# Kernel tuning notes

Hardware: AMD Instinct MI355X
Metric: run time of the kernel (lower is better)

Reference implementation:

```python
import jax, jax.numpy as jnp
import numpy as np

NEG_SLOPE = 0.2  # PyG GATConv leaky_relu slope


def gat_conv(x, src, dst, W, a_src, a_dst, bias, heads, out_ch, concat, n_nodes):
    # x: [N, in], W: [heads*out_ch, in], a_src/a_dst: [heads, out_ch]
    h = (x @ W.T).reshape(n_nodes, heads, out_ch)          # [N,H,C]
    alpha_src = (h * a_src).sum(-1)                         # [N,H]
    alpha_dst = (h * a_dst).sum(-1)                         # [N,H]
    e = jax.nn.leaky_relu(alpha_src[src] + alpha_dst[dst], NEG_SLOPE)  # [E,H]
    # segment softmax over incoming edges of each dst node (self-loops ensure non-empty)
    m = jax.ops.segment_max(e, dst, num_segments=n_nodes)
    e = jnp.exp(e - m[dst])
    s = jax.ops.segment_sum(e, dst, num_segments=n_nodes)
    alpha = e / (s[dst] + 1e-16)                            # [E,H]
    msg = h[src] * alpha[:, :, None]                        # [E,H,C]
    out = jax.ops.segment_sum(msg, dst, num_segments=n_nodes)  # [N,H,C]
    out = out.reshape(n_nodes, heads * out_ch) if concat else out.mean(axis=1)
    return out + bias


def setup_inputs() -> dict:
    key = jax.random.key(0)
    ks = jax.random.split(key, 16)
    N, E, IN, HID, OUT, H1, H2 = 10000, 160000, 256, 32, 32, 8, 10
    inp = {
        "x": jax.random.normal(ks[0], (N, IN), dtype=jnp.float32),
        "edge_index": jax.random.randint(ks[1], (2, E), 0, N, dtype=jnp.int64),
        # GATConv 1: in=256 -> 8 heads x 32
        "W1": jax.random.normal(ks[2], (H1 * HID, IN), dtype=jnp.float32) * 0.05,
        "a1s": jax.random.normal(ks[3], (H1, HID), dtype=jnp.float32) * 0.05,
        "a1d": jax.random.normal(ks[4], (H1, HID), dtype=jnp.float32) * 0.05,
        "b1": jnp.zeros((H1 * HID,), dtype=jnp.float32),
        # GATConv 2: in=256 -> 8 heads x 32
        "W2": jax.random.normal(ks[5], (H1 * HID, H1 * HID), dtype=jnp.float32) * 0.05,
        "a2s": jax.random.normal(ks[6], (H1, HID), dtype=jnp.float32) * 0.05,
        "a2d": jax.random.normal(ks[7], (H1, HID), dtype=jnp.float32) * 0.05,
        "b2": jnp.zeros((H1 * HID,), dtype=jnp.float32),
        # GATConv 3: in=256 -> 10 heads x 32, concat=False (mean)
        "W3": jax.random.normal(ks[8], (H2 * OUT, H1 * HID), dtype=jnp.float32) * 0.05,
        "a3s": jax.random.normal(ks[9], (H2, OUT), dtype=jnp.float32) * 0.05,
        "a3d": jax.random.normal(ks[10], (H2, OUT), dtype=jnp.float32) * 0.05,
        "b3": jnp.zeros((OUT,), dtype=jnp.float32),
        # residual projections
        "P1W": jax.random.normal(ks[11], (H1 * HID, IN), dtype=jnp.float32) * 0.05,
        "P1b": jnp.zeros((H1 * HID,), dtype=jnp.float32),
        "P3W": jax.random.normal(ks[12], (OUT, H1 * HID), dtype=jnp.float32) * 0.05,
        "P3b": jnp.zeros((OUT,), dtype=jnp.float32),
    }
    return inp


def reference(x, edge_index, W1, a1s, a1d, b1, W2, a2s, a2d, b2,
              W3, a3s, a3d, b3, P1W, P1b, P3W, P3b):
    N = x.shape[0]
    loop = jnp.arange(N, dtype=edge_index.dtype)
    src = jnp.concatenate([edge_index[0], loop])  # PyG adds self-loops by default
    dst = jnp.concatenate([edge_index[1], loop])

    identity1 = x @ P1W.T + P1b
    h = gat_conv(x, src, dst, W1, a1s, a1d, b1, 8, 32, True, N)
    h = jax.nn.elu(h) + identity1  # dropout inactive in eval

    identity2 = h
    h2 = gat_conv(h, src, dst, W2, a2s, a2d, b2, 8, 32, True, N)
    h = jax.nn.elu(h2) + identity2

    identity3 = h @ P3W.T + P3b
    h3 = gat_conv(h, src, dst, W3, a3s, a3d, b3, 10, 32, False, N)
    return h3 + identity3
```

## Files before the change

kernel.cpp:

```cpp
#include <hip/hip_runtime.h>
#include <hip/hip_bf16.h>

typedef __hip_bfloat16 bf16;
typedef __attribute__((ext_vector_type(8))) short bf16x8;
typedef __attribute__((ext_vector_type(4))) short bf16x4;
typedef __attribute__((ext_vector_type(4))) float f32x4;


static __device__ __forceinline__ float bf2f(bf16 v) { return __bfloat162float(v); }
static __device__ __forceinline__ float bf2fs(short v) {
    unsigned int u = ((unsigned int)(unsigned short)v) << 16;
    return __builtin_bit_cast(float, u);
}
static __device__ __forceinline__ short f2bfs(float f) {
    bf16 b = __float2bfloat16(f);
    return __builtin_bit_cast(short, b);
}
static __device__ __forceinline__ float loadf(const void* p, size_t i, int isf32) {
    return isf32 ? ((const float*)p)[i] : bf2f(((const bf16*)p)[i]);
}
static __device__ __forceinline__ int get_isf32(const int* flags) {
    return (flags[0] | (flags[2] == 0)) ? 1 : 0;
}

__global__ void k_zero(int* __restrict__ flags, int* __restrict__ cnt, int N) {
    int i = blockIdx.x * blockDim.x + threadIdx.x;
    if (i < 4) flags[i] = 0;
    for (; i < N; i += gridDim.x * blockDim.x) cnt[i] = 0;
}

__global__ void k_detect(const unsigned short* __restrict__ xu, const int* __restrict__ ew,
                         int* __restrict__ flags, int nx, int ne2, int bx) {
    __shared__ int lf[3];
    if (threadIdx.x < 3) lf[threadIdx.x] = 0;
    __syncthreads();
    if ((int)blockIdx.x < bx) {
        for (int i = blockIdx.x * 256 + threadIdx.x; i < nx; i += bx * 256) {
            unsigned short v = xu[i];
            if ((v & 0x7F80u) == 0x7F80u) lf[0] = 1;
            if (((i & 1) == 0) && v != 0) lf[2] = 1;
        }
    } else {
        int nb = gridDim.x - bx;
        for (int i = (blockIdx.x - bx) * 256 + threadIdx.x; i < ne2; i += nb * 256) {
            if ((i & 1) && ew[i] != 0) lf[1] = 1;
        }
    }
    __syncthreads();
    if (threadIdx.x == 0) {
        if (lf[0]) atomicOr(&flags[0], 1);
        if (lf[1]) atomicOr(&flags[1], 1);
        if (lf[2]) atomicOr(&flags[2], 1);
    }
}

static __device__ __forceinline__ void cast8(const void* src, bf16* dst, int i8, int isf32) {
    if (isf32) {
        f32x4 a = ((const f32x4*)src)[2 * i8];
        f32x4 b = ((const f32x4*)src)[2 * i8 + 1];
        bf16x8 o;
        o[0] = f2bfs(a[0]); o[1] = f2bfs(a[1]); o[2] = f2bfs(a[2]); o[3] = f2bfs(a[3]);
        o[4] = f2bfs(b[0]); o[5] = f2bfs(b[1]); o[6] = f2bfs(b[2]); o[7] = f2bfs(b[3]);
        ((bf16x8*)dst)[i8] = o;
    } else {
        ((bf16x8*)dst)[i8] = ((const bf16x8*)src)[i8];
    }
}

__global__ void k_cast_all(const void* s0, bf16* d0, int c0,
                           const void* s1, bf16* d1, int c1,
                           const void* s2, bf16* d2, int c2,
                           const void* s3, bf16* d3, int c3,
                           const void* s4, bf16* d4, int c4,
                           const void* s5, bf16* d5, int c5,
                           const int* __restrict__ flags) {
    int t = blockIdx.x * blockDim.x + threadIdx.x;
    int isf32 = get_isf32(flags);
    if (t < c0) { cast8(s0, d0, t, isf32); return; } t -= c0;
    if (t < c1) { cast8(s1, d1, t, isf32); return; } t -= c1;
    if (t < c2) { cast8(s2, d2, t, isf32); return; } t -= c2;
    if (t < c3) { cast8(s3, d3, t, isf32); return; } t -= c3;
    if (t < c4) { cast8(s4, d4, t, isf32); return; } t -= c4;
    if (t < c5) { cast8(s5, d5, t, isf32); }
}

__global__ void k_norm_count(const int* __restrict__ w, const int* __restrict__ flags,
                             int* __restrict__ s, int* __restrict__ d,
                             int* __restrict__ cnt, int E) {
    int e = blockIdx.x * blockDim.x + threadIdx.x;
    if (e >= E) return;
    int sv, dv;
    if (flags[1] == 0) {
        sv = w[2 * (size_t)e];
        dv = w[2 * (size_t)E + 2 * (size_t)e];
    } else {
        sv = w[e];
        dv = w[(size_t)E + e];
    }
    s[e] = sv;
    d[e] = dv;
    atomicAdd(&cnt[dv], 1);
}

__global__ void k_scan(int* __restrict__ cnt, int* __restrict__ row_ptr, int N) {
    __shared__ int part[1024];
    int tid = threadIdx.x;
    int vpt = (N + 1023) >> 10;
    int i0 = tid * vpt;
    int i1 = i0 + vpt; if (i1 > N) i1 = N;
    int s = 0;
    for (int i = i0; i < i1; ++i) s += cnt[i] + 1;
    part[tid] = s;
    __syncthreads();
    for (int off = 1; off < 1024; off <<= 1) {
        int t = (tid >= off) ? part[tid - off] : 0;
        __syncthreads();
        part[tid] += t;
        __syncthreads();
    }
    int run = (tid == 0) ? 0 : part[tid - 1];
    for (int i = i0; i < i1; ++i) {
        int c = cnt[i] + 1;
        cnt[i] = run;
        run += c;
        row_ptr[i + 1] = run;
    }
    if (tid == 0) row_ptr[0] = 0;
}

__global__ void k_fill(const int* __restrict__ edst, int* __restrict__ cursor,
                       const int* __restrict__ row_ptr, int* __restrict__ csr_e,
                       int E, int N) {
    int e = blockIdx.x * blockDim.x + threadIdx.x;
    if (e < E) {
        int d = edst[e];
        int pos = atomicAdd(&cursor[d], 1);
        csr_e[pos] = e;
    } else if (e < E + N) {
        int d = e - E;
        csr_e[row_ptr[d + 1] - 1] = e;
    }
}

template<int NT>
__global__ void k_gemm_split(const bf16* __restrict__ A, const bf16* __restrict__ W,
                             const void* __restrict__ bias1, const int* __restrict__ flags,
                             bf16* __restrict__ out0, int S0, int ld0,
                             float* __restrict__ out1, int ld1, int n1,
                             int M, int Fo, int K,
                             const void* __restrict__ aS, const void* __restrict__ aD,
                             float* __restrict__ asrc, float* __restrict__ adst, int H) {
    int wid = threadIdx.x >> 6;
    int lane = threadIdx.x & 63;
    int mrow = blockIdx.x * 64 + wid * 16;
    if (mrow >= M) return;
    int ncol = blockIdx.y * (NT * 16);
    int r = lane & 15, g = lane >> 4;

    f32x4 acc[NT];
#pragma unroll
    for (int t = 0; t < NT; ++t) acc[t] = (f32x4){0.f, 0.f, 0.f, 0.f};

    const bf16* arow = A + (size_t)(mrow + r) * K + g * 8;
    const bf16* wbase = W + (size_t)(ncol + r) * K + g * 8;
    for (int k0 = 0; k0 < K; k0 += 32) {
        bf16x8 af = *(const bf16x8*)(arow + k0);
#pragma unroll
        for (int t = 0; t < NT; ++t) {
            bf16x8 bfr = *(const bf16x8*)(wbase + (size_t)t * 16 * K + k0);
            acc[t] = __builtin_amdgcn_mfma_f32_16x16x32_bf16(af, bfr, acc[t], 0, 0, 0);
        }
    }
    int isf32 = get_isf32(flags);

#pragma unroll
    for (int t = 0; t < NT; ++t) {
        int n = ncol + t * 16 + r;
        bool is0 = n < S0;
        int jc = n - S0;
        float bv = (!is0 && jc < n1 && bias1) ? loadf(bias1, jc, isf32) : 0.f;
#pragma unroll
        for (int j = 0; j < 4; ++j) {
            int m = mrow + 4 * g + j;
            float v = acc[t][j] + bv;
            if (is0) out0[(size_t)m * ld0 + n] = __float2bfloat16(v);
            else if (jc < n1) out1[(size_t)m * ld1 + jc] = v;
        }
    }

    if (aS && ncol < S0) {
        float ps[2][4], pd[2][4];
#pragma unroll
        for (int hb = 0; hb < 2; ++hb)
#pragma unroll
            for (int j = 0; j < 4; ++j) { ps[hb][j] = 0.f; pd[hb][j] = 0.f; }
#pragma unroll
        for (int t = 0; t < NT; ++t) {
            int col = ncol + t * 16 + r;
            float asv = loadf(aS, col, isf32);
            float adv = loadf(aD, col, isf32);
#pragma unroll
            for (int j = 0; j < 4; ++j) {
                ps[t >> 1][j] += acc[t][j] * asv;
                pd[t >> 1][j] += acc[t][j] * adv;
            }
        }
#pragma unroll
        for (int mk = 1; mk <= 8; mk <<= 1) {
#pragma unroll
            for (int hb = 0; hb < 2; ++hb)
#pragma unroll
                for (int j = 0; j < 4; ++j) {
                    ps[hb][j] += __shfl_xor(ps[hb][j], mk);
                    pd[hb][j] += __shfl_xor(pd[hb][j], mk);
                }
        }
        if (r == 0) {
            int hA = ncol >> 5, hB = hA + 1;
#pragma unroll
            for (int j = 0; j < 4; ++j) {
                int m = mrow + 4 * g + j;
                asrc[(size_t)m * H + hA] = ps[0][j];
                asrc[(size_t)m * H + hB] = ps[1][j];
                adst[(size_t)m * H + hA] = pd[0][j];
                adst[(size_t)m * H + hB] = pd[1][j];
            }
        }
    }
}

#define CAP 96
__global__ void k_fused_agg(const bf16* __restrict__ hlin,
                            const float* __restrict__ asrc, const float* __restrict__ adst,
                            const int* __restrict__ esrc, const int* __restrict__ row_ptr,
                            const int* __restrict__ csr_e,
                            const void* __restrict__ bias, const float* __restrict__ ident,
                            void* __restrict__ out, bf16* __restrict__ outb,
                            const int* __restrict__ flags,
                            int E, int N, int H, int mode) {
    __shared__ float el[4][CAP * 10];
    __shared__ int   ssrc[4][CAP];
    __shared__ float idn[4][10];
    int wid = threadIdx.x >> 6, lane = threadIdx.x & 63;
    int d = blockIdx.x * 4 + wid;
    bool active = d < N;
    int isf32 = get_isf32(flags);
    int F = H * 32;
    int nj = (F + 255) >> 8;
    int lo = 0, deg = 0;
    if (active) { lo = row_ptr[d]; deg = row_ptr[d + 1] - lo; }
    bool fast = deg <= CAP;

    if (active && fast) {
        int EC = 64 / H;
        int h = lane % H, ei = lane / H;
        float ad = adst[(size_t)d * H + h];
        for (int base = 0; base < deg; base += EC) {
            int p = base + ei;
            if (ei < EC && p < deg) {
                int e = csr_e[lo + p];
                int s = (e < E) ? esrc[e] : (e - E);
                float v = asrc[(size_t)s * H + h] + ad;
                v = (v > 0.f) ? v : 0.2f * v;
                el[wid][p * H + h] = v;
                if (h == 0) ssrc[wid][p] = s;
            }
        }
    }
    __syncthreads();
    if (active && fast) {
        if (H == 8) {
            int h = lane & 7, sub = lane >> 3;
            float m = -1e30f;
            for (int p = sub; p < deg; p += 8) m = fmaxf(m, el[wid][p * 8 + h]);
            m = fmaxf(m, __shfl_xor(m, 8));
            m = fmaxf(m, __shfl_xor(m, 16));
            m = fmaxf(m, __shfl_xor(m, 32));
            float den = 0.f;
            for (int p = sub; p < deg; p += 8) {
                float t = __expf(el[wid][p * 8 + h] - m);
                el[wid][p * 8 + h] = t;
                den += t;
            }
            den += __shfl_xor(den, 8);
            den += __shfl_xor(den, 16);
            den += __shfl_xor(den, 32);
            if (lane < 8) idn[wid][lane] = 1.f / (den + 1e-16f);
        } else if (lane < H) {
            float m = -1e30f;
            for (int p = 0; p < deg; ++p) m = fmaxf(m, el[wid][p * H + lane]);
            float den = 0.f;
            for (int p = 0; p < deg; ++p) {
                float t = __expf(el[wid][p * H + lane] - m);
                el[wid][p * H + lane] = t;
                den += t;
            }
            idn[wid][lane] = 1.f / (den + 1e-16f);
        }
    }
    __syncthreads();
    if (!active) return;

    if (mode == 1 && fast) {
        int g = lane & 15, q = lane >> 4;
        int f0 = g * 16;
        f32x4 a0 = {0.f,0.f,0.f,0.f}, a1 = {0.f,0.f,0.f,0.f};
        f32x4 a2 = {0.f,0.f,0.f,0.f}, a3 = {0.f,0.f,0.f,0.f};
        for (int p = q; p < deg; p += 4) {
            int s = ssrc[wid][p];
            const bf16* hp = hlin + (size_t)s * 256 + f0;
            bf16x8 h0 = *(const bf16x8*)hp;
            bf16x8 h1 = *(const bf16x8*)(hp + 8);
            float w = el[wid][p * 8 + (g >> 1)];
#pragma unroll
            for (int k = 0; k < 4; ++k) {
                a0[k] += w * bf2fs(h0[k]);
                a1[k] += w * bf2fs(h0[4 + k]);
                a2[k] += w * bf2fs(h1[k]);
                a3[k] += w * bf2fs(h1[4 + k]);
            }
        }
#pragma unroll
        for (int k = 0; k < 4; ++k) {
            a0[k] += __shfl_xor(a0[k], 16); a1[k] += __shfl_xor(a1[k], 16);
            a2[k] += __shfl_xor(a2[k], 16); a3[k] += __shfl_xor(a3[k], 16);
            a0[k] += __shfl_xor(a0[k], 32); a1[k] += __shfl_xor(a1[k], 32);
            a2[k] += __shfl_xor(a2[k], 32); a3[k] += __shfl_xor(a3[k], 32);
        }
        if (lane < 16) {
            float inv = idn[wid][g >> 1];
            const float* idp = ident + (size_t)d * 256 + f0;
            float* o = (float*)out + (size_t)d * 256 + f0;
            bf16* ob = outb + (size_t)d * 256 + f0;
            f32x4 av[4] = {a0, a1, a2, a3};
            bf16x8 obv0, obv1;
#pragma unroll
            for (int i = 0; i < 4; ++i) {
                f32x4 idv = *(const f32x4*)(idp + 4 * i);
                f32x4 ov;
#pragma unroll
                for (int k = 0; k < 4; ++k) {
                    float v = av[i][k] * inv + loadf(bias, f0 + 4 * i + k, isf32);
                    v = (v > 0.f) ? v : (__expf(v) - 1.f);
                    v += idv[k];
                    ov[k] = v;
                    if (i < 2) obv0[4 * i + k] = f2bfs(v);
                    else       obv1[4 * (i - 2) + k] = f2bfs(v);
                }
                *(f32x4*)(o + 4 * i) = ov;
            }
            *(bf16x8*)ob = obv0;
            *(bf16x8*)(ob + 8) = obv1;
        }
        return;
    }

    f32x4 acc[2] = {(f32x4){0.f,0.f,0.f,0.f}, (f32x4){0.f,0.f,0.f,0.f}};
    if (fast) {
        f32x4 accB[2] = {(f32x4){0.f,0.f,0.f,0.f}, (f32x4){0.f,0.f,0.f,0.f}};
        int hj0 = lane >> 3;
        int p = 0;
        for (; p + 1 < deg; p += 2) {
            int s0 = ssrc[wid][p], s1 = ssrc[wid][p + 1];
            bf16x4 h00 = *(const bf16x4*)(hlin + (size_t)s0 * F + lane * 4);
            bf16x4 h10 = *(const bf16x4*)(hlin + (size_t)s1 * F + lane * 4);
            float w00 = el[wid][p * H + hj0];
            float w10 = el[wid][(p + 1) * H + hj0];
#pragma unroll
            for (int k = 0; k < 4; ++k) {
                acc[0][k]  += w00 * bf2fs(h00[k]);
                accB[0][k] += w10 * bf2fs(h10[k]);
            }
            if (nj == 2 && lane < 16) {
                int f1 = 256 + lane * 4;
                bf16x4 h01 = *(const bf16x4*)(hlin + (size_t)s0 * F + f1);
                bf16x4 h11 = *(const bf16x4*)(hlin + (size_t)s1 * F + f1);
                float w01 = el[wid][p * H + 8 + hj0];
                float w11 = el[wid][(p + 1) * H + 8 + hj0];
#pragma unroll
                for (int k = 0; k < 4; ++k) {
                    acc[1][k]  += w01 * bf2fs(h01[k]);
                    accB[1][k] += w11 * bf2fs(h11[k]);
                }
            }
        }
        if (p < deg) {
            int s0 = ssrc[wid][p];
            bf16x4 h00 = *(const bf16x4*)(hlin + (size_t)s0 * F + lane * 4);
            float w00 = el[wid][p * H + hj0];
#pragma unroll
            for (int k = 0; k < 4; ++k) acc[0][k] += w00 * bf2fs(h00[k]);
            if (nj == 2 && lane < 16) {
                int f1 = 256 + lane * 4;
                bf16x4 h01 = *(const bf16x4*)(hlin + (size_t)s0 * F + f1);
                float w01 = el[wid][p * H + 8 + hj0];
#pragma unroll
                for (int k = 0; k < 4; ++k) acc[1][k] += w01 * bf2fs(h01[k]);
            }
        }
#pragma unroll
        for (int j = 0; j < 2; ++j)
#pragma unroll
            for (int k = 0; k < 4; ++k) acc[j][k] += accB[j][k];
        {
            float inv0 = idn[wid][hj0];
#pragma unroll
            for (int k = 0; k < 4; ++k) acc[0][k] *= inv0;
            if (nj == 2 && lane < 16) {
                float inv1 = idn[wid][8 + hj0];
#pragma unroll
                for (int k = 0; k < 4; ++k) acc[1][k] *= inv1;
            }
        }
    } else {
        for (int j = 0; j < nj; ++j) {
            int f0 = (lane + 64 * j) * 4;
            if (f0 >= F) continue;
            int hj = f0 >> 5;
            float ad = adst[(size_t)d * H + hj];
            float m = -1e30f;
            for (int p = 0; p < deg; ++p) {
                int e = csr_e[lo + p];
                int s = (e < E) ? esrc[e] : (e - E);
                float v = asrc[(size_t)s * H + hj] + ad;
                v = (v > 0.f) ? v : 0.2f * v;
                m = fmaxf(m, v);
            }
            float den = 0.f;
            f32x4 a4 = {0.f, 0.f, 0.f, 0.f};
            for (int p = 0; p < deg; ++p) {
                int e = csr_e[lo + p];
                int s = (e < E) ? esrc[e] : (e - E);
                float v = asrc[(size_t)s * H + hj] + ad;
                v = (v > 0.f) ? v : 0.2f * v;
                float t = __expf(v - m);
                den += t;
                bf16x4 hv = *(const bf16x4*)(hlin + (size_t)s * F + f0);
                for (int k = 0; k < 4; ++k) a4[k] += t * bf2fs(hv[k]);
            }
            float inv = 1.f / (den + 1e-16f);
            for (int k = 0; k < 4; ++k) acc[j][k] = a4[k] * inv;
        }
    }
    if (mode == 1) {
        float* o = (float*)out;
        int f0 = lane * 4;
        f32x4 idv = *(const f32x4*)(ident + (size_t)d * F + f0);
        f32x4 ov;
        bf16x4 ob;
#pragma unroll
        for (int k = 0; k < 4; ++k) {
            float v = acc[0][k] + loadf(bias, f0 + k, isf32);
            v = (v > 0.f) ? v : (__expf(v) - 1.f);
            v += idv[k];
            ov[k] = v;
            ob[k] = f2bfs(v);
        }
        *(f32x4*)(o + (size_t)d * F + f0) = ov;
        *(bf16x4*)(outb + (size_t)d * F + f0) = ob;
    } else {
        float* scratch = &el[wid][0];
#pragma unroll
        for (int j = 0; j < 2; ++j) {
            int f0 = (lane + 64 * j) * 4;
            if (j < nj && f0 < F) {
#pragma unroll
                for (int k = 0; k < 4; ++k) scratch[f0 + k] = acc[j][k];
            }
        }
        if (lane < 32) {
            float s = 0.f;
            for (int h = 0; h < H; ++h) s += scratch[h * 32 + lane];
            float v = s * (1.f / (float)H) + loadf(bias, lane, isf32)
                    + ident[(size_t)d * 32 + lane];
            if (isf32) ((float*)out)[(size_t)d * 32 + lane] = v;
            else ((bf16*)out)[(size_t)d * 32 + lane] = __float2bfloat16(v);
        }
    }
}

extern "C" void kernel_launch(void* const* d_in, const int* in_sizes, int n_in,
                              void* d_out, int out_size, void* d_ws, size_t ws_size,
                              hipStream_t stream) {
    const int IN = 256, C = 32;
    const int N = in_sizes[0] / IN;
    const int E = in_sizes[1] / 2;
    const int ET = E + N;

    const void* x    = d_in[0];
    const int*  edge = (const int*)d_in[1];
    const void* W1 = d_in[2];
    const void* a1s = d_in[3];
    const void* a1d = d_in[4];
    const void* b1 = d_in[5];
    const void* W2 = d_in[6];
    const void* a2s = d_in[7];
    const void* a2d = d_in[8];
    const void* b2 = d_in[9];
    const void* W3 = d_in[10];
    const void* a3s = d_in[11];
    const void* a3d = d_in[12];
    const void* b3 = d_in[13];
    const void* P1W = d_in[14];
    const void* P1b = d_in[15];
    const void* P3W = d_in[16];
    const void* P3b = d_in[17];

    char* ws = (char*)d_ws;
    size_t off = 0;
    auto alloc = [&](size_t bytes) -> void* {
        void* p = ws + off;
        off = (off + bytes + 255) & ~(size_t)255;
        return p;
    };
    bf16* fxb   = (bf16*)alloc((size_t)N * 256 * 2);
    bf16* fyb   = (bf16*)alloc((size_t)N * 256 * 2);
    bf16* fhb   = (bf16*)alloc((size_t)N * 320 * 2);
    float* fy   = (float*)alloc((size_t)N * 256 * 4);
    float* fid  = (float*)alloc((size_t)N * 256 * 4);
    float* fasrc = (float*)alloc((size_t)N * 10 * 4);
    float* fadst = (float*)alloc((size_t)N * 10 * 4);
    bf16* wc1   = (bf16*)alloc((size_t)512 * 256 * 2);
    bf16* wb2   = (bf16*)alloc((size_t)256 * 256 * 2);
    bf16* wc3   = (bf16*)alloc((size_t)384 * 256 * 2);
    int*  isrc  = (int*)alloc((size_t)E * 4);
    int*  idst  = (int*)alloc((size_t)E * 4);
    int*  irow  = (int*)alloc((size_t)(N + 1) * 4);
    int*  icur  = (int*)alloc((size_t)N * 4);
    int*  icsr  = (int*)alloc((size_t)ET * 4);
    int*  flags = (int*)alloc(4 * 4);
    (void)ws_size;

    auto cdiv = [](int a, int b) { return (a + b - 1) / b; };

    k_zero<<<cdiv(N, 256), 256, 0, stream>>>(flags, icur, N);

    int nprobe_x = (N * 256 < 16384) ? N * 256 : 16384;
    int nprobe_e = (2 * E < 8192) ? 2 * E : 8192;
    int bx = cdiv(nprobe_x, 256) < 16 ? cdiv(nprobe_x, 256) : 16;
    int be = cdiv(nprobe_e, 256) < 8 ? cdiv(nprobe_e, 256) : 8;
    k_detect<<<bx + be, 256, 0, stream>>>(
        (const unsigned short*)x, edge, flags, nprobe_x, nprobe_e, bx);

    int c_x = N * 256 / 8, c_w = 256 * 256 / 8, c_w3 = 320 * 256 / 8, c_p3 = 32 * 256 / 8;
    int ctot = c_x + 3 * c_w + c_w3 + c_p3;
    k_cast_all<<<cdiv(ctot, 256), 256, 0, stream>>>(
        x, fxb, c_x,
        W1, wc1, c_w,
        P1W, wc1 + (size_t)256 * 256, c_w,
        W2, wb2, c_w,
        W3, wc3, c_w3,
        P3W, wc3 + (size_t)320 * 256, c_p3,
        flags);

    k_norm_count<<<cdiv(E, 256), 256, 0, stream>>>(edge, flags, isrc, idst, icur, E);
    k_scan<<<1, 1024, 0, stream>>>(icur, irow, N);
    k_fill<<<cdiv(ET, 256), 256, 0, stream>>>(idst, icur, irow, icsr, E, N);

    int gx = cdiv(N, 64);
    int ga = cdiv(N, 4);

    {
        int H = 8;
        k_gemm_split<4><<<dim3(gx, 8), 256, 0, stream>>>(
            fxb, wc1, P1b, flags, fhb, 256, 256, fid, 256, 256, N, 512, 256,
            a1s, a1d, fasrc, fadst, H);
        k_fused_agg<<<ga, 256, 0, stream>>>(fhb, fasrc, fadst, isrc, irow, icsr, b1, fid, fy, fyb, flags, E, N, H, 1);
    }
    {
        int H = 8;
        k_gemm_split<4><<<dim3(gx, 4), 256, 0, stream>>>(
            fyb, wb2, nullptr, flags, fhb, 256, 256, nullptr, 0, 0, N, 256, 256,
            a2s, a2d, fasrc, fadst, H);
        k_fused_agg<<<ga, 256, 0, stream>>>(fhb, fasrc, fadst, isrc, irow, icsr, b2, fy, fy, fyb, flags, E, N, H, 1);
    }
    {
        int H = 10;
        k_gemm_split<4><<<dim3(gx, 6), 256, 0, stream>>>(
            fyb, wc3, P3b, flags, fhb, 320, 320, fid, 32, 32, N, 384, 256,
            a3s, a3d, fasrc, fadst, H);
        k_fused_agg<<<ga, 256, 0, stream>>>(fhb, fasrc, fadst, isrc, irow, icsr, b3, fid, d_out, nullptr, flags, E, N, H, 2);
    }
}
```

Before: 215.5 us.

## Store residual activations in bf16 and add vectorized mode-2 aggregation path

Residual and identity tensors now live in bf16 instead of fp32. The GEMM writes its projection output as bf16, and the aggregation kernel reads bf16 identities and no longer writes a separate fp32 activation copy. This cuts the global memory traffic of writing and reading the large per-node feature buffers. A new fast path for the final mean-over-heads layer splits each wave into four groups of sixteen lanes, each group gathering a different edge with wide 16-byte loads, then reduces across groups with shuffles. The cost is lower precision in the residual path, which may move results closer to the tolerance limit.

```diff
diff --git a/kernel.cpp b/kernel.cpp
--- a/kernel.cpp
+++ b/kernel.cpp
@@ -146,7 +146,7 @@
 __global__ void k_gemm_split(const bf16* __restrict__ A, const bf16* __restrict__ W,
                              const void* __restrict__ bias1, const int* __restrict__ flags,
                              bf16* __restrict__ out0, int S0, int ld0,
-                             float* __restrict__ out1, int ld1, int n1,
+                             bf16* __restrict__ out1, int ld1, int n1,
                              int M, int Fo, int K,
                              const void* __restrict__ aS, const void* __restrict__ aD,
                              float* __restrict__ asrc, float* __restrict__ adst, int H) {
@@ -184,7 +184,7 @@
             int m = mrow + 4 * g + j;
             float v = acc[t][j] + bv;
             if (is0) out0[(size_t)m * ld0 + n] = __float2bfloat16(v);
-            else if (jc < n1) out1[(size_t)m * ld1 + jc] = v;
+            else if (jc < n1) out1[(size_t)m * ld1 + jc] = __float2bfloat16(v);
         }
     }
 
@@ -234,7 +234,7 @@
                             const float* __restrict__ asrc, const float* __restrict__ adst,
                             const int* __restrict__ esrc, const int* __restrict__ row_ptr,
                             const int* __restrict__ csr_e,
-                            const void* __restrict__ bias, const float* __restrict__ ident,
+                            const void* __restrict__ bias, const bf16* __restrict__ identb,
                             void* __restrict__ out, bf16* __restrict__ outb,
                             const int* __restrict__ flags,
                             int E, int N, int H, int mode) {
@@ -329,25 +329,23 @@
         }
         if (lane < 16) {
             float inv = idn[wid][g >> 1];
-            const float* idp = ident + (size_t)d * 256 + f0;
-            float* o = (float*)out + (size_t)d * 256 + f0;
+            const bf16* idp = identb + (size_t)d * 256 + f0;
+            bf16x8 id0 = *(const bf16x8*)idp;
+            bf16x8 id1 = *(const bf16x8*)(idp + 8);
             bf16* ob = outb + (size_t)d * 256 + f0;
             f32x4 av[4] = {a0, a1, a2, a3};
             bf16x8 obv0, obv1;
 #pragma unroll
             for (int i = 0; i < 4; ++i) {
-                f32x4 idv = *(const f32x4*)(idp + 4 * i);
-                f32x4 ov;
 #pragma unroll
                 for (int k = 0; k < 4; ++k) {
                     float v = av[i][k] * inv + loadf(bias, f0 + 4 * i + k, isf32);
                     v = (v > 0.f) ? v : (__expf(v) - 1.f);
-                    v += idv[k];
-                    ov[k] = v;
-                    if (i < 2) obv0[4 * i + k] = f2bfs(v);
-                    else       obv1[4 * (i - 2) + k] = f2bfs(v);
+                    int e8 = 4 * i + k;
+                    v += bf2fs((e8 < 8) ? id0[e8] : id1[e8 - 8]);
+                    if (i < 2) obv0[e8] = f2bfs(v);
+                    else       obv1[e8 - 8] = f2bfs(v);
                 }
-                *(f32x4*)(o + 4 * i) = ov;
             }
             *(bf16x8*)ob = obv0;
             *(bf16x8*)(ob + 8) = obv1;
@@ -355,108 +353,103 @@
         return;
     }
 
+    if (mode == 2 && fast) {
+        int g = lane & 15, q = lane >> 4;
+        int f0 = g * 16;
+        int f1 = 256 + g * 4;
+        f32x4 a0 = {0.f,0.f,0.f,0.f}, a1 = {0.f,0.f,0.f,0.f};
+        f32x4 a2 = {0.f,0.f,0.f,0.f}, a3 = {0.f,0.f,0.f,0.f};
+        f32x4 a4 = {0.f,0.f,0.f,0.f};
+        for (int p = q; p < deg; p += 4) {
+            int s = ssrc[wid][p];
+            const bf16* hp = hlin + (size_t)s * 320;
+            bf16x8 h0 = *(const bf16x8*)(hp + f0);
+            bf16x8 h1 = *(const bf16x8*)(hp + f0 + 8);
+            bf16x4 h2 = *(const bf16x4*)(hp + f1);
+            float w0 = el[wid][p * 10 + (g >> 1)];
+            float w2 = el[wid][p * 10 + 8 + (g >> 3)];
+#pragma unroll
+            for (int k = 0; k < 4; ++k) {
+                a0[k] += w0 * bf2fs(h0[k]);
+                a1[k] += w0 * bf2fs(h0[4 + k]);
+                a2[k] += w0 * bf2fs(h1[k]);
+                a3[k] += w0 * bf2fs(h1[4 + k]);
+                a4[k] += w2 * bf2fs(h2[k]);
+            }
+        }
+#pragma unroll
+        for (int k = 0; k < 4; ++k) {
+            a0[k] += __shfl_xor(a0[k], 16); a1[k] += __shfl_xor(a1[k], 16);
+            a2[k] += __shfl_xor(a2[k], 16); a3[k] += __shfl_xor(a3[k], 16);
+            a4[k] += __shfl_xor(a4[k], 16);
+            a0[k] += __shfl_xor(a0[k], 32); a1[k] += __shfl_xor(a1[k], 32);
+            a2[k] += __shfl_xor(a2[k], 32); a3[k] += __shfl_xor(a3[k], 32);
+            a4[k] += __shfl_xor(a4[k], 32);
+        }
+        float* scratch = &el[wid][0];
+        if (lane < 16) {
+            float inv0 = idn[wid][g >> 1];
+            float inv2 = idn[wid][8 + (g >> 3)];
+#pragma unroll
+            for (int k = 0; k < 4; ++k) {
+                scratch[f0 + k]      = a0[k] * inv0;
+                scratch[f0 + 4 + k]  = a1[k] * inv0;
+                scratch[f0 + 8 + k]  = a2[k] * inv0;
+                scratch[f0 + 12 + k] = a3[k] * inv0;
+                scratch[f1 + k]      = a4[k] * inv2;
+            }
+        }
+        if (lane < 32) {
+            float s = 0.f;
+#pragma unroll
+            for (int h = 0; h < 10; ++h) s += scratch[h * 32 + lane];
+            float v = s * 0.1f + loadf(bias, lane, isf32)
+                    + bf2f(identb[(size_t)d * 32 + lane]);
+            if (isf32) ((float*)out)[(size_t)d * 32 + lane] = v;
+            else ((bf16*)out)[(size_t)d * 32 + lane] = __float2bfloat16(v);
+        }
+        return;
+    }
+
     f32x4 acc[2] = {(f32x4){0.f,0.f,0.f,0.f}, (f32x4){0.f,0.f,0.f,0.f}};
-    if (fast) {
-        f32x4 accB[2] = {(f32x4){0.f,0.f,0.f,0.f}, (f32x4){0.f,0.f,0.f,0.f}};
-        int hj0 = lane >> 3;
-        int p = 0;
-        for (; p + 1 < deg; p += 2) {
-            int s0 = ssrc[wid][p], s1 = ssrc[wid][p + 1];
-            bf16x4 h00 = *(const bf16x4*)(hlin + (size_t)s0 * F + lane * 4);
-            bf16x4 h10 = *(const bf16x4*)(hlin + (size_t)s1 * F + lane * 4);
-            float w00 = el[wid][p * H + hj0];
-            float w10 = el[wid][(p + 1) * H + hj0];
-#pragma unroll
-            for (int k = 0; k < 4; ++k) {
-                acc[0][k]  += w00 * bf2fs(h00[k]);
-                accB[0][k] += w10 * bf2fs(h10[k]);
-            }
-            if (nj == 2 && lane < 16) {
-                int f1 = 256 + lane * 4;
-                bf16x4 h01 = *(const bf16x4*)(hlin + (size_t)s0 * F + f1);
-                bf16x4 h11 = *(const bf16x4*)(hlin + (size_t)s1 * F + f1);
-                float w01 = el[wid][p * H + 8 + hj0];
-                float w11 = el[wid][(p + 1) * H + 8 + hj0];
-#pragma unroll
-                for (int k = 0; k < 4; ++k) {
-                    acc[1][k]  += w01 * bf2fs(h01[k]);
-                    accB[1][k] += w11 * bf2fs(h11[k]);
-                }
-            }
-        }
-        if (p < deg) {
-            int s0 = ssrc[wid][p];
-            bf16x4 h00 = *(const bf16x4*)(hlin + (size_t)s0 * F + lane * 4);
-            float w00 = el[wid][p * H + hj0];
-#pragma unroll
-            for (int k = 0; k < 4; ++k) acc[0][k] += w00 * bf2fs(h00[k]);
-            if (nj == 2 && lane < 16) {
-                int f1 = 256 + lane * 4;
-                bf16x4 h01 = *(const bf16x4*)(hlin + (size_t)s0 * F + f1);
-                float w01 = el[wid][p * H + 8 + hj0];
-#pragma unroll
-                for (int k = 0; k < 4; ++k) acc[1][k] += w01 * bf2fs(h01[k]);
-            }
-        }
-#pragma unroll
-        for (int j = 0; j < 2; ++j)
-#pragma unroll
-            for (int k = 0; k < 4; ++k) acc[j][k] += accB[j][k];
-        {
-            float inv0 = idn[wid][hj0];
-#pragma unroll
-            for (int k = 0; k < 4; ++k) acc[0][k] *= inv0;
-            if (nj == 2 && lane < 16) {
-                float inv1 = idn[wid][8 + hj0];
-#pragma unroll
-                for (int k = 0; k < 4; ++k) acc[1][k] *= inv1;
-            }
-        }
-    } else {
-        for (int j = 0; j < nj; ++j) {
-            int f0 = (lane + 64 * j) * 4;
-            if (f0 >= F) continue;
-            int hj = f0 >> 5;
-            float ad = adst[(size_t)d * H + hj];
-            float m = -1e30f;
-            for (int p = 0; p < deg; ++p) {
-                int e = csr_e[lo + p];
-                int s = (e < E) ? esrc[e] : (e - E);
-                float v = asrc[(size_t)s * H + hj] + ad;
-                v = (v > 0.f) ? v : 0.2f * v;
-                m = fmaxf(m, v);
-            }
-            float den = 0.f;
-            f32x4 a4 = {0.f, 0.f, 0.f, 0.f};
-            for (int p = 0; p < deg; ++p) {
-                int e = csr_e[lo + p];
-                int s = (e < E) ? esrc[e] : (e - E);
-                float v = asrc[(size_t)s * H + hj] + ad;
-                v = (v > 0.f) ? v : 0.2f * v;
-                float t = __expf(v - m);
-                den += t;
-                bf16x4 hv = *(const bf16x4*)(hlin + (size_t)s * F + f0);
-                for (int k = 0; k < 4; ++k) a4[k] += t * bf2fs(hv[k]);
-            }
-            float inv = 1.f / (den + 1e-16f);
-            for (int k = 0; k < 4; ++k) acc[j][k] = a4[k] * inv;
-        }
+    for (int j = 0; j < nj; ++j) {
+        int f0 = (lane + 64 * j) * 4;
+        if (f0 >= F) continue;
+        int hj = f0 >> 5;
+        float ad = adst[(size_t)d * H + hj];
+        float m = -1e30f;
+        for (int p = 0; p < deg; ++p) {
+            int e = csr_e[lo + p];
+            int s = (e < E) ? esrc[e] : (e - E);
+            float v = asrc[(size_t)s * H + hj] + ad;
+            v = (v > 0.f) ? v : 0.2f * v;
+            m = fmaxf(m, v);
+        }
+        float den = 0.f;
+        f32x4 a4 = {0.f, 0.f, 0.f, 0.f};
+        for (int p = 0; p < deg; ++p) {
+            int e = csr_e[lo + p];
+            int s = (e < E) ? esrc[e] : (e - E);
+            float v = asrc[(size_t)s * H + hj] + ad;
+            v = (v > 0.f) ? v : 0.2f * v;
+            float t = __expf(v - m);
+            den += t;
+            bf16x4 hv = *(const bf16x4*)(hlin + (size_t)s * F + f0);
+            for (int k = 0; k < 4; ++k) a4[k] += t * bf2fs(hv[k]);
+        }
+        float inv = 1.f / (den + 1e-16f);
+        for (int k = 0; k < 4; ++k) acc[j][k] = a4[k] * inv;
     }
     if (mode == 1) {
-        float* o = (float*)out;
         int f0 = lane * 4;
-        f32x4 idv = *(const f32x4*)(ident + (size_t)d * F + f0);
-        f32x4 ov;
         bf16x4 ob;
 #pragma unroll
         for (int k = 0; k < 4; ++k) {
             float v = acc[0][k] + loadf(bias, f0 + k, isf32);
             v = (v > 0.f) ? v : (__expf(v) - 1.f);
-            v += idv[k];
-            ov[k] = v;
+            v += bf2f(identb[(size_t)d * F + f0 + k]);
             ob[k] = f2bfs(v);
         }
-        *(f32x4*)(o + (size_t)d * F + f0) = ov;
         *(bf16x4*)(outb + (size_t)d * F + f0) = ob;
     } else {
         float* scratch = &el[wid][0];
@@ -472,7 +465,7 @@
             float s = 0.f;
             for (int h = 0; h < H; ++h) s += scratch[h * 32 + lane];
             float v = s * (1.f / (float)H) + loadf(bias, lane, isf32)
-                    + ident[(size_t)d * 32 + lane];
+                    + bf2f(identb[(size_t)d * 32 + lane]);
             if (isf32) ((float*)out)[(size_t)d * 32 + lane] = v;
             else ((bf16*)out)[(size_t)d * 32 + lane] = __float2bfloat16(v);
         }
@@ -516,8 +509,7 @@
     bf16* fxb   = (bf16*)alloc((size_t)N * 256 * 2);
     bf16* fyb   = (bf16*)alloc((size_t)N * 256 * 2);
     bf16* fhb   = (bf16*)alloc((size_t)N * 320 * 2);
-    float* fy   = (float*)alloc((size_t)N * 256 * 4);
-    float* fid  = (float*)alloc((size_t)N * 256 * 4);
+    bf16* fidb  = (bf16*)alloc((size_t)N * 256 * 2);
     float* fasrc = (float*)alloc((size_t)N * 10 * 4);
     float* fadst = (float*)alloc((size_t)N * 10 * 4);
     bf16* wc1   = (bf16*)alloc((size_t)512 * 256 * 2);
@@ -563,22 +555,25 @@
     {
         int H = 8;
         k_gemm_split<4><<<dim3(gx, 8), 256, 0, stream>>>(
-            fxb, wc1, P1b, flags, fhb, 256, 256, fid, 256, 256, N, 512, 256,
+            fxb, wc1, P1b, flags, fhb, 256, 256, fidb, 256, 256, N, 512, 256,
             a1s, a1d, fasrc, fadst, H);
-        k_fused_agg<<<ga, 256, 0, stream>>>(fhb, fasrc, fadst, isrc, irow, icsr, b1, fid, fy, fyb, flags, E, N, H, 1);
+        k_fused_agg<<<ga, 256, 0, stream>>>(fhb, fasrc, fadst, isrc, irow, icsr,
+                                            b1, fidb, nullptr, fyb, flags, E, N, H, 1);
     }
     {
         int H = 8;
         k_gemm_split<4><<<dim3(gx, 4), 256, 0, stream>>>(
             fyb, wb2, nullptr, flags, fhb, 256, 256, nullptr, 0, 0, N, 256, 256,
             a2s, a2d, fasrc, fadst, H);
-        k_fused_agg<<<ga, 256, 0, stream>>>(fhb, fasrc, fadst, isrc, irow, icsr, b2, fy, fy, fyb, flags, E, N, H, 1);
+        k_fused_agg<<<ga, 256, 0, stream>>>(fhb, fasrc, fadst, isrc, irow, icsr,
+                                            b2, fyb, nullptr, fyb, flags, E, N, H, 1);
     }
     {
         int H = 10;
         k_gemm_split<4><<<dim3(gx, 6), 256, 0, stream>>>(
-            fyb, wc3, P3b, flags, fhb, 320, 320, fid, 32, 32, N, 384, 256,
+            fyb, wc3, P3b, flags, fhb, 320, 320, fidb, 32, 32, N, 384, 256,
             a3s, a3d, fasrc, fadst, H);
-        k_fused_agg<<<ga, 256, 0, stream>>>(fhb, fasrc, fadst, isrc, irow, icsr, b3, fid, d_out, nullptr, flags, E, N, H, 2);
-    }
-}
+        k_fused_agg<<<ga, 256, 0, stream>>>(fhb, fasrc, fadst, isrc, irow, icsr,
+                                            b3, fidb, d_out, nullptr, flags, E, N, H, 2);
+    }
+}
```

Measured after the change: 202.9 us. 5.9% less time.
